# Optimization experiments

Measured on AMD Instinct MI355X. Metric: run time of the kernel, lower is better.

Reference implementation:

```python
import jax, jax.numpy as jnp
import numpy as np

IN_F, HID, OUT_F = 227, 1024, 227
BATCH, SEQ_LEN = 256, 100
COND_NUM, GT_NUM = 5, 5


def _condition_lst(seq_len, condition_num=COND_NUM, groundtruth_num=GT_NUM):
    gt = np.ones((100, groundtruth_num))
    con = np.zeros((100, condition_num))
    lst = np.concatenate((gt, con), 1).reshape(-1)
    return lst[:seq_len].astype(bool)


def _lstm_cell(x, h, c, Wih, Whh, bih, bhh):
    gates = x @ Wih.T + bih + h @ Whh.T + bhh  # [B, 4H]
    i, f, g, o = jnp.split(gates, 4, axis=-1)
    c_new = jax.nn.sigmoid(f) * c + jax.nn.sigmoid(i) * jnp.tanh(g)
    h_new = jax.nn.sigmoid(o) * jnp.tanh(c_new)
    return h_new, c_new


def setup_inputs() -> dict:
    key = jax.random.key(0)
    ks = jax.random.split(key, 16)
    s = 0.03
    inp = {"real_seq": jax.random.normal(ks[0], (BATCH, SEQ_LEN, IN_F), jnp.float32)}
    shapes = {
        "Wih1": (4 * HID, IN_F), "Whh1": (4 * HID, HID), "bih1": (4 * HID,), "bhh1": (4 * HID,),
        "Wih2": (4 * HID, HID), "Whh2": (4 * HID, HID), "bih2": (4 * HID,), "bhh2": (4 * HID,),
        "Wih3": (4 * HID, HID), "Whh3": (4 * HID, HID), "bih3": (4 * HID,), "bhh3": (4 * HID,),
        "Wd": (OUT_F, HID), "bd": (OUT_F,),
    }
    for i, (name, shp) in enumerate(shapes.items()):
        inp[name] = jax.random.normal(ks[i + 1], shp, jnp.float32) * s
    return inp


def reference(real_seq, Wih1, Whh1, bih1, bhh1, Wih2, Whh2, bih2, bhh2,
              Wih3, Whh3, bih3, bhh3, Wd, bd):
    batch, seq_len, _ = real_seq.shape
    cond = jnp.asarray(_condition_lst(seq_len))  # [T] bool, True -> teacher forcing
    zeros_h = jnp.zeros((batch, HID), real_seq.dtype)
    out0 = jnp.zeros((batch, OUT_F), real_seq.dtype)
    carry0 = (zeros_h, zeros_h, zeros_h, zeros_h, zeros_h, zeros_h, out0)

    def step(carry, xs):
        h0, h1, h2, c0, c1, c2, prev_out = carry
        gt_frame, use_gt = xs
        in_frame = jnp.where(use_gt, gt_frame, prev_out)
        # NOTE: faithful to the original quirk — lstm2/lstm3 consume the OLD
        # h0 / h1 (pre-update), not the freshly computed ones.
        h0n, c0n = _lstm_cell(in_frame, h0, c0, Wih1, Whh1, bih1, bhh1)
        h1n, c1n = _lstm_cell(h0, h1, c1, Wih2, Whh2, bih2, bhh2)
        h2n, c2n = _lstm_cell(h1, h2, c2, Wih3, Whh3, bih3, bhh3)
        out_frame = h2n @ Wd.T + bd
        return (h0n, h1n, h2n, c0n, c1n, c2n, out_frame), out_frame

    xs = (jnp.transpose(real_seq, (1, 0, 2)), cond)  # [T,B,F], [T]
    _, out_frames = jax.lax.scan(step, carry0, xs)   # [T,B,OUT_F]
    out_seq = jnp.transpose(out_frames, (1, 0, 2)).reshape(batch, seq_len * OUT_F)
    return out_seq
```

## Files before the change

kernel.cpp:

```cpp
#include <hip/hip_runtime.h>
#include <cstdint>

typedef _Float16 f16;
typedef _Float16 f16x8 __attribute__((ext_vector_type(8)));
typedef float    f32x4 __attribute__((ext_vector_type(4)));

#define DINL __device__ __forceinline__

static constexpr int HID = 1024;
static constexpr int NG  = 4096;
static constexpr int BB  = 256;
static constexpr int TT  = 100;
static constexpr int KX  = 256;
static constexpr size_t MSZ = (size_t)NG * HID;

static constexpr size_t OFF_PACKW5 = 0;
static constexpr size_t OFF_W1D    = OFF_PACKW5 + 5*MSZ*2;
static constexpr size_t OFF_WIH1   = OFF_W1D   + MSZ*2;
static constexpr size_t OFF_WD     = OFF_WIH1  + (size_t)NG*KX*2;
static constexpr size_t OFF_XPAD   = OFF_WD    + (size_t)256*HID*2;
static constexpr size_t OFF_BIAS   = OFF_XPAD  + (size_t)TT*BB*KX*2;
static constexpr size_t OFF_C      = OFF_BIAS  + (size_t)4*NG*4;
static constexpr size_t OFF_HBUF   = OFF_C     + (size_t)3*BB*HID*4;
static constexpr size_t OFF_H2Z    = OFF_HBUF  + (size_t)4*BB*HID*2;
static constexpr size_t OFF_H2ALL  = OFF_H2Z   + (size_t)BB*HID*2;

DINL size_t fpo(int n, int k, int NCH){
  return ((((size_t)(n>>4)*NCH + (k>>6))*2 + ((k>>5)&1)) << 9)
       + ((size_t)((n&15) | (((k>>3)&3) << 4)) << 3) + (k&7);
}

DINL void async16(void* lds, const void* g){
  auto lp = reinterpret_cast<__attribute__((address_space(3))) unsigned int*>(
      reinterpret_cast<uintptr_t>(lds));
  auto gp = reinterpret_cast<const __attribute__((address_space(1))) unsigned int*>(
      reinterpret_cast<uintptr_t>(g));
  __builtin_amdgcn_global_load_lds(gp, lp, 16, 0, 0);
}

DINL f16x8 ldsr128(unsigned a){
  f16x8 r;
  asm volatile("ds_read_b128 %0, %1" : "=v"(r) : "v"(a));
  return r;
}

DINL f16x8 gload(const void* addr){
  f16x8 r;
  asm volatile("global_load_dwordx4 %0, %1, off"
    : "=v"(r) : "v"(addr));
  return r;
}

DINL f32x4 mfma8(f16x8 a, f16x8 b, f32x4 c){
  return __builtin_amdgcn_mfma_f32_16x16x32_f16(a, b, c, 0, 0, 0);
}

DINL float sigf(float x){
  x = fminf(fmaxf(x, -30.f), 30.f);
  return __fdividef(1.f, 1.f + __expf(-x));
}
DINL float tanh_fast(float x){
  x = fminf(fmaxf(x, -15.f), 15.f);
  float t = __expf(2.f*x);
  return __fdividef(t - 1.f, t + 1.f);
}


__global__ void k_pack5(const float* W0, const float* W1, const float* W2,
                        const float* W3, const float* W4, char* ws)
{
  f16* dst = (f16*)(ws + OFF_PACKW5);
  const int mat = blockIdx.y;
  const float* src = mat==0?W0 : mat==1?W1 : mat==2?W2 : mat==3?W3 : W4;
  int tid = blockIdx.x*256 + threadIdx.x;
  int n = tid >> 7, kc = tid & 127;
  int r = ((n&3) << 10) + (n >> 2);
  const float* s = src + (size_t)r*HID + kc*8;
  f16x8 o;
  #pragma unroll
  for (int i = 0; i < 8; i++) o[i] = (f16)s[i];
  int nt = n >> 4, cch = kc >> 3, kw = (kc >> 2) & 1, quad = kc & 3;
  size_t off = ((((size_t)nt*16 + cch)*2 + kw) << 9)
             + ((size_t)((n&15) | (quad<<4)) << 3);
  *(f16x8*)(dst + (size_t)mat*MSZ + off) = o;
}

__global__ void k_packwih1(const float* __restrict__ Wih1, char* ws){
  f16* dst = (f16*)(ws + OFF_WIH1);
  int n = blockIdx.x, k = threadIdx.x;
  int r = ((n&3) << 10) + (n >> 2);
  dst[fpo(n, k, 4)] = (k < 227) ? (f16)Wih1[(size_t)r*227 + k] : (f16)0.f;
}

__global__ void k_packwd(const float* __restrict__ Wd, char* ws){
  f16* dst = (f16*)(ws + OFF_WD);
  int idx = blockIdx.x*256 + threadIdx.x;
  int o = idx >> 7, k8 = idx & 127;
  f16x8 v;
  #pragma unroll
  for (int e = 0; e < 8; e++)
    v[e] = (o < 227) ? (f16)Wd[(size_t)o*HID + k8*8 + e] : (f16)0.f;
  size_t off = ((((size_t)(o>>4)*16 + (k8>>3))*2 + ((k8>>2)&1)) << 9)
             + ((size_t)((o&15) | ((k8&3)<<4)) << 3);
  *(f16x8*)(dst + off) = v;
}

__global__ void k_packwdt(const float* __restrict__ Wd, char* ws){
  f16* dst = (f16*)(ws + OFF_H2ALL);
  int h = blockIdx.x, o = threadIdx.x;
  dst[fpo(h, o, 4)] = (o < 227) ? (f16)Wd[(size_t)o*HID + h] : (f16)0.f;
}

__global__ void k_xpad(const float* __restrict__ seq, char* ws){
  f16* dst = (f16*)(ws + OFF_XPAD);
  int idx = blockIdx.x*256 + threadIdx.x;
  int t = idx >> 13, rem = idx & 8191, b = rem >> 5, k8 = rem & 31;
  f16x8 v;
  #pragma unroll
  for (int e = 0; e < 8; e++){
    int k = k8*8 + e;
    v[e] = (k < 227) ? (f16)seq[(size_t)b*22700 + (size_t)t*227 + k] : (f16)0.f;
  }
  size_t off = ((((size_t)(b>>4)*4 + (k8>>3))*2 + ((k8>>2)&1)) << 9)
             + ((size_t)((b&15) | ((k8&3)<<4)) << 3);
  *(f16x8*)(dst + (size_t)t*BB*KX + off) = v;
}

__global__ void k_bias(const float* bih1, const float* bhh1, const float* bih2, const float* bhh2,
                       const float* bih3, const float* bhh3, const float* Wih1, const float* bd,
                       char* ws)
{
  int n = blockIdx.x*256 + threadIdx.x;
  if (n >= NG) return;
  int r = ((n&3) << 10) + (n >> 2);
  float* b = (float*)(ws + OFF_BIAS);
  float bf = bih1[r] + bhh1[r];
  float s = 0.f;
  for (int o = 0; o < 227; o++) s += Wih1[(size_t)r*227 + o] * bd[o];
  b[n]        = bf;
  b[NG + n]   = bf + s;
  b[2*NG + n] = bih2[r] + bhh2[r];
  b[3*NG + n] = bih3[r] + bhh3[r];
}

__global__ __launch_bounds__(256) void k_w1d(char* ws)
{
  const int w = threadIdx.x >> 6, lane = threadIdx.x & 63;
  const int n0 = blockIdx.x*128, m0 = blockIdx.y*128;
  const f16* Af = (const f16*)(ws + OFF_WIH1);
  const f16* Bf = (const f16*)(ws + OFF_H2ALL);
  f16* W1D = (f16*)(ws + OFF_W1D);
  const int m_w = m0 + (w>>1)*64, n_w = n0 + (w&1)*64;
  const int vl = lane*8;

  f32x4 acc[4][4];
  f32x4 zero = {0.f, 0.f, 0.f, 0.f};
  #pragma unroll
  for (int i = 0; i < 4; i++)
    #pragma unroll
    for (int j = 0; j < 4; j++) acc[i][j] = zero;

  for (int c = 0; c < 4; c++){
    f16x8 av[4][2], bv[4][2];
    #pragma unroll
    for (int ti = 0; ti < 4; ti++)
      #pragma unroll
      for (int kw = 0; kw < 2; kw++)
        av[ti][kw] = *(const f16x8*)(Af + ((((size_t)((m_w>>4)+ti)*4 + c)*2 + kw) << 9) + vl);
    #pragma unroll
    for (int tj = 0; tj < 4; tj++)
      #pragma unroll
      for (int kw = 0; kw < 2; kw++)
        bv[tj][kw] = *(const f16x8*)(Bf + ((((size_t)((n_w>>4)+tj)*4 + c)*2 + kw) << 9) + vl);
    #pragma unroll
    for (int kw = 0; kw < 2; kw++)
      #pragma unroll
      for (int ti = 0; ti < 4; ti++)
        #pragma unroll
        for (int tj = 0; tj < 4; tj++)
          acc[ti][tj] = mfma8(av[ti][kw], bv[tj][kw], acc[ti][tj]);
  }

  const int quad = lane>>4, c15 = lane&15;
  #pragma unroll
  for (int tj = 0; tj < 4; tj++){
    int col = n_w + tj*16 + c15;
    #pragma unroll
    for (int ti = 0; ti < 4; ti++){
      f32x4 v = acc[ti][tj];
      #pragma unroll
      for (int r = 0; r < 4; r++){
        int m = m_w + ti*16 + quad*4 + r;
        W1D[fpo(m, col, 16)] = (f16)v[r];
      }
    }
  }
}

__global__ __launch_bounds__(512, 2) void k_step(char* __restrict__ ws, int t, int use_gt)
{
  __shared__ __align__(16) char lds[65536];
  const int w = threadIdx.x >> 6, lane = threadIdx.x & 63;
  const int col0 = blockIdx.x*64, layer = blockIdx.y;

  const f16* packW = (const f16*)(ws + OFF_PACKW5);
  const f16* W1D   = (const f16*)(ws + OFF_W1D);
  const f16* WIH1  = (const f16*)(ws + OFF_WIH1);
  const f16* XP    = (const f16*)(ws + OFF_XPAD) + (size_t)t*BB*KX;
  const float* biasb = (const float*)(ws + OFF_BIAS);
  float* Cst = (float*)(ws + OFF_C);
  f16* HB  = (f16*)(ws + OFF_HBUF);
  f16* H2Z = (f16*)(ws + OFF_H2Z);
  f16* H2A = (f16*)(ws + OFF_H2ALL);

  const int pr = t & 1, pw = pr ^ 1;
  const f16* h0p = HB + (size_t)(pr*2 + 0)*BB*HID;
  const f16* h1p = HB + (size_t)(pr*2 + 1)*BB*HID;
  const f16* h2p = (t == 0) ? H2Z : (H2A + (size_t)(t-1)*BB*HID);

  const f16 *A0, *A1, *B0, *B1; int K1;
  const float* biasp; f16* hout; float* cptr;
  if (layer == 0){
    A0 = h0p; B0 = packW;
    if (use_gt){ A1 = XP;  B1 = WIH1; K1 = KX;  biasp = biasb; }
    else       { A1 = h2p; B1 = W1D;  K1 = HID; biasp = biasb + NG; }
    hout = HB + (size_t)(pw*2 + 0)*BB*HID; cptr = Cst;
  } else if (layer == 1){
    A0 = h0p; B0 = packW + MSZ;  A1 = h1p; B1 = packW + 2*MSZ; K1 = HID;
    biasp = biasb + 2*NG; hout = HB + (size_t)(pw*2 + 1)*BB*HID; cptr = Cst + (size_t)BB*HID;
  } else {
    A0 = h1p; B0 = packW + 3*MSZ; A1 = h2p; B1 = packW + 4*MSZ; K1 = HID;
    biasp = biasb + 3*NG; hout = H2A + (size_t)t*BB*HID; cptr = Cst + (size_t)2*BB*HID;
  }
  const int ncmax = 16 + (K1 >> 6);
  const int NCH1  = K1 >> 6;

  const int m_w = w*32, c15 = lane&15, quad = lane>>4;
  const unsigned vl16 = (unsigned)(lane * 16);
  const unsigned ldsBase = (unsigned)(uintptr_t)lds;

  const char* a0b[2]; const char* a1b[2];
  #pragma unroll
  for (int ti = 0; ti < 2; ti++){
    a0b[ti] = (const char*)A0 + (size_t)(2*w + ti)*16*2048   + (size_t)lane*16;
    a1b[ti] = (const char*)A1 + (size_t)(2*w + ti)*NCH1*2048 + (size_t)lane*16;
  }
  const char* b0u = (const char*)B0 + (size_t)((col0>>4) + (w>>1))*16*2048   + (size_t)(w&1)*1024 + (size_t)lane*16;
  const char* b1u = (const char*)B1 + (size_t)((col0>>4) + (w>>1))*NCH1*2048 + (size_t)(w&1)*1024 + (size_t)lane*16;

  auto issueB = [&](int ci){
    const char* s = (ci < 16) ? (b0u + (size_t)ci*2048) : (b1u + (size_t)(ci-16)*2048);
    async16(lds + (ci & 7)*8192 + w*1024, s);
  };
  auto abase = [&](int ci, int ti)->const char*{
    return (ci < 16) ? (a0b[ti] + (size_t)ci*2048) : (a1b[ti] + (size_t)(ci-16)*2048);
  };

  f32x4 acc[2][4];
  f32x4 zero = {0.f, 0.f, 0.f, 0.f};
  #pragma unroll
  for (int i = 0; i < 2; i++)
    #pragma unroll
    for (int j = 0; j < 4; j++) acc[i][j] = zero;

  f16x8 akA[4], akB[4];

#define ISSUEA(CI, AK)                                           \
  { const char* _b0 = abase((CI), 0);                            \
    const char* _b1 = abase((CI), 1);                            \
    AK[0] = gload(_b0);                                          \
    AK[1] = gload(_b0 + 1024);                                   \
    AK[2] = gload(_b1);                                          \
    AK[3] = gload(_b1 + 1024); }

#define WAITA(N, AK) asm volatile("s_waitcnt vmcnt(" #N ")"      \
    : "+v"(AK[0]), "+v"(AK[1]), "+v"(AK[2]), "+v"(AK[3]))

#define BMM(CI, AK)                                              \
  { const unsigned sb = ldsBase + (unsigned)(((CI)&7)*8192) + vl16; \
    f16x8 b00 = ldsr128(sb);        f16x8 b10 = ldsr128(sb+2048);   \
    f16x8 b20 = ldsr128(sb+4096);   f16x8 b30 = ldsr128(sb+6144);   \
    f16x8 b01 = ldsr128(sb+1024);   f16x8 b11 = ldsr128(sb+3072);   \
    f16x8 b21 = ldsr128(sb+5120);   f16x8 b31 = ldsr128(sb+7168);   \
    asm volatile("s_waitcnt lgkmcnt(4)"                          \
      : "+v"(b00), "+v"(b10), "+v"(b20), "+v"(b30));             \
    acc[0][0] = mfma8(AK[0], b00, acc[0][0]);                    \
    acc[0][1] = mfma8(AK[0], b10, acc[0][1]);                    \
    acc[0][2] = mfma8(AK[0], b20, acc[0][2]);                    \
    acc[0][3] = mfma8(AK[0], b30, acc[0][3]);                    \
    acc[1][0] = mfma8(AK[2], b00, acc[1][0]);                    \
    acc[1][1] = mfma8(AK[2], b10, acc[1][1]);                    \
    acc[1][2] = mfma8(AK[2], b20, acc[1][2]);                    \
    acc[1][3] = mfma8(AK[2], b30, acc[1][3]);                    \
    asm volatile("s_waitcnt lgkmcnt(0)"                          \
      : "+v"(b01), "+v"(b11), "+v"(b21), "+v"(b31));             \
    acc[0][0] = mfma8(AK[1], b01, acc[0][0]);                    \
    acc[0][1] = mfma8(AK[1], b11, acc[0][1]);                    \
    acc[0][2] = mfma8(AK[1], b21, acc[0][2]);                    \
    acc[0][3] = mfma8(AK[1], b31, acc[0][3]);                    \
    acc[1][0] = mfma8(AK[3], b01, acc[1][0]);                    \
    acc[1][1] = mfma8(AK[3], b11, acc[1][1]);                    \
    acc[1][2] = mfma8(AK[3], b21, acc[1][2]);                    \
    acc[1][3] = mfma8(AK[3], b31, acc[1][3]); }

#define ITERI(CI, VMN, AK)  { WAITA(VMN, AK); BMM(CI, AK); ISSUEA((CI)+2, AK); }
#define ITERN(CI, VMN, AK)  { WAITA(VMN, AK); BMM(CI, AK); }

  issueB(0); issueB(1); issueB(2); issueB(3);
  issueB(4); issueB(5); issueB(6); issueB(7);
  ISSUEA(0, akA); ISSUEA(1, akB);
  asm volatile("s_waitcnt vmcnt(4)" ::: "memory");
  __builtin_amdgcn_s_barrier();
  __builtin_amdgcn_sched_barrier(0);

  ITERI(0, 4, akA) ITERI(1, 4, akB) ITERI(2, 4, akA) ITERI(3, 4, akB)

  for (int h = 1; h <= (ncmax >> 2) - 2; ++h){
    __builtin_amdgcn_s_barrier();
    __builtin_amdgcn_sched_barrier(0);
    const int cb = 4*(h+1);
    issueB(cb); issueB(cb+1); issueB(cb+2); issueB(cb+3);
    const int c = 4*h;
    ITERI(c,   8, akA) ITERI(c+1, 8, akB) ITERI(c+2, 4, akA) ITERI(c+3, 4, akB)
  }

  __builtin_amdgcn_s_barrier();
  __builtin_amdgcn_sched_barrier(0);
  { const int c = ncmax - 4;
    ITERI(c,   4, akA) ITERI(c+1, 4, akB) ITERN(c+2, 4, akA) ITERN(c+3, 0, akB) }

#undef ITERN
#undef ITERI
#undef BMM
#undef WAITA
#undef ISSUEA

  const int gl = lane&3, sbase = lane&60;
  #pragma unroll
  for (int tj = 0; tj < 4; tj++){
    const int ncol = col0 + tj*16 + c15;
    const int unit = ncol >> 2;
    const float bn = biasp[ncol];
    float cp[8];
    #pragma unroll
    for (int ti = 0; ti < 2; ti++)
      #pragma unroll
      for (int r = 0; r < 4; r++)
        cp[ti*4 + r] = cptr[(size_t)(m_w + ti*16 + quad*4 + r)*HID + unit];
    #pragma unroll
    for (int ti = 0; ti < 2; ti++){
      f32x4 v = acc[ti][tj];
      #pragma unroll
      for (int r = 0; r < 4; r++){
        float x   = v[r] + bn;
        float act = (gl == 2) ? tanh_fast(x) : sigf(x);
        float iv = __shfl(act, sbase);
        float fv = __shfl(act, sbase + 1);
        float gv = __shfl(act, sbase + 2);
        float ov = __shfl(act, sbase + 3);
        float cn = fmaf(fv, cp[ti*4 + r], iv*gv);
        float hn = ov * tanh_fast(cn);
        int m = m_w + ti*16 + quad*4 + r;
        if (gl == 0)      cptr[(size_t)m*HID + unit] = cn;
        else if (gl == 1) hout[fpo(m, unit, 16)] = (f16)hn;
      }
    }
  }
}

__global__ __launch_bounds__(256) void k_final(const char* __restrict__ ws,
                                               const float* __restrict__ bd,
                                               float* __restrict__ dout)
{
  const int w = threadIdx.x >> 6, lane = threadIdx.x & 63;
  const int n0 = blockIdx.x*128, m0 = blockIdx.y*128;
  const char* Bf = ws + OFF_WD;
  const int m_w = m0 + (w>>1)*64, n_w = n0 + (w&1)*64;
  const char* Af = ws + OFF_H2ALL + (size_t)(m_w >> 8)*BB*HID*2;
  const int vl = lane*16;

  f32x4 acc[4][4];
  f32x4 zero = {0.f, 0.f, 0.f, 0.f};
  #pragma unroll
  for (int i = 0; i < 4; i++)
    #pragma unroll
    for (int j = 0; j < 4; j++) acc[i][j] = zero;

  for (int c = 0; c < 16; c++){
    f16x8 av[4][2], bv[4][2];
    #pragma unroll
    for (int ti = 0; ti < 4; ti++){
      const char* b = Af + (((size_t)(((m_w & 255) >> 4) + ti)*16 + c) << 11) + vl;
      av[ti][0] = *(const f16x8*)(b);
      av[ti][1] = *(const f16x8*)(b + 1024);
    }
    #pragma unroll
    for (int tj = 0; tj < 4; tj++){
      const char* b = Bf + (((size_t)((n_w >> 4) + tj)*16 + c) << 11) + vl;
      bv[tj][0] = *(const f16x8*)(b);
      bv[tj][1] = *(const f16x8*)(b + 1024);
    }
    #pragma unroll
    for (int kw = 0; kw < 2; kw++)
      #pragma unroll
      for (int ti = 0; ti < 4; ti++)
        #pragma unroll
        for (int tj = 0; tj < 4; tj++)
          acc[ti][tj] = mfma8(av[ti][kw], bv[tj][kw], acc[ti][tj]);
  }

  const int quad = lane>>4, c15 = lane&15;
  #pragma unroll
  for (int tj = 0; tj < 4; tj++){
    int o = n_w + tj*16 + c15;
    bool valid = (o < 227);
    float bn = valid ? bd[o] : 0.f;
    #pragma unroll
    for (int ti = 0; ti < 4; ti++){
      f32x4 v = acc[ti][tj];
      #pragma unroll
      for (int r = 0; r < 4; r++){
        int m = m_w + ti*16 + quad*4 + r;
        if (valid){
          int tt = m >> 8, b = m & 255;
          dout[(size_t)b*22700 + (size_t)tt*227 + o] = v[r] + bn;
        }
      }
    }
  }
}

extern "C" void kernel_launch(void* const* d_in, const int* in_sizes, int n_in,
                              void* d_out, int out_size, void* d_ws, size_t ws_size,
                              hipStream_t stream)
{
  (void)in_sizes; (void)n_in; (void)out_size; (void)ws_size;
  const float* seq  = (const float*)d_in[0];
  const float* Wih1 = (const float*)d_in[1];
  const float* Whh1 = (const float*)d_in[2];
  const float* bih1 = (const float*)d_in[3];
  const float* bhh1 = (const float*)d_in[4];
  const float* Wih2 = (const float*)d_in[5];
  const float* Whh2 = (const float*)d_in[6];
  const float* bih2 = (const float*)d_in[7];
  const float* bhh2 = (const float*)d_in[8];
  const float* Wih3 = (const float*)d_in[9];
  const float* Whh3 = (const float*)d_in[10];
  const float* bih3 = (const float*)d_in[11];
  const float* bhh3 = (const float*)d_in[12];
  const float* Wd   = (const float*)d_in[13];
  const float* bd   = (const float*)d_in[14];
  char* ws = (char*)d_ws;

  (void)hipMemsetAsync(ws + OFF_C,    0, (size_t)3*BB*HID*4, stream);
  (void)hipMemsetAsync(ws + OFF_HBUF, 0, (size_t)2*BB*HID*2, stream);
  (void)hipMemsetAsync(ws + OFF_H2Z,  0, (size_t)BB*HID*2,   stream);

  k_pack5   <<<dim3(2048, 5), dim3(256), 0, stream>>>(Whh1, Wih2, Whh2, Wih3, Whh3, ws);
  k_packwih1<<<dim3(4096),    dim3(256), 0, stream>>>(Wih1, ws);
  k_packwd  <<<dim3(128),     dim3(256), 0, stream>>>(Wd, ws);
  k_packwdt <<<dim3(1024),    dim3(256), 0, stream>>>(Wd, ws);
  k_xpad    <<<dim3(3200),    dim3(256), 0, stream>>>(seq, ws);
  k_bias    <<<dim3(16),      dim3(256), 0, stream>>>(bih1, bhh1, bih2, bhh2, bih3, bhh3, Wih1, bd, ws);
  k_w1d     <<<dim3(8, 32),   dim3(256), 0, stream>>>(ws);

  for (int t = 0; t < TT; t++){
    int ug = ((t % 10) < 5) ? 1 : 0;
    k_step<<<dim3(64, 3), dim3(512), 0, stream>>>(ws, t, ug);
  }

  k_final<<<dim3(2, 200), dim3(256), 0, stream>>>((const char*)ws, bd, (float*)d_out);
}
```

Before: 2.918 ms.

## Deepen GEMM pipeline with triple-buffered A registers and prefetched LDS B fragments

Restructures the recurrent GEMM main loop so A fragments are loaded three chunks ahead (three register sets instead of two) and B fragments for the next chunk are read from LDS into a second register set while the MFMAs for the current chunk run. The loop is unrolled into 12-chunk blocks with barriers and B async copies placed every four chunks. The aim is to hide global-load and LDS-read latency behind the MFMAs. In exchange it raises VGPR pressure, which may lower occupancy, and the hand-counted waitcnt values make it fragile if ncmax-8 is not a multiple of 12.

```diff
diff --git a/kernel.cpp b/kernel.cpp
--- a/kernel.cpp
+++ b/kernel.cpp
@@ -263,7 +263,8 @@
     #pragma unroll
     for (int j = 0; j < 4; j++) acc[i][j] = zero;
 
-  f16x8 akA[4], akB[4];
+  f16x8 A0r[4], A1r[4], A2r[4];
+  f16x8 F0[8], F1[8];
 
 #define ISSUEA(CI, AK)                                           \
   { const char* _b0 = abase((CI), 0);                            \
@@ -273,66 +274,84 @@
     AK[2] = gload(_b1);                                          \
     AK[3] = gload(_b1 + 1024); }
 
-#define WAITA(N, AK) asm volatile("s_waitcnt vmcnt(" #N ")"      \
+#define WAITA_N(LIT, AK) asm volatile("s_waitcnt vmcnt(" #LIT ")" \
     : "+v"(AK[0]), "+v"(AK[1]), "+v"(AK[2]), "+v"(AK[3]))
 
-#define BMM(CI, AK)                                              \
-  { const unsigned sb = ldsBase + (unsigned)(((CI)&7)*8192) + vl16; \
-    f16x8 b00 = ldsr128(sb);        f16x8 b10 = ldsr128(sb+2048);   \
-    f16x8 b20 = ldsr128(sb+4096);   f16x8 b30 = ldsr128(sb+6144);   \
-    f16x8 b01 = ldsr128(sb+1024);   f16x8 b11 = ldsr128(sb+3072);   \
-    f16x8 b21 = ldsr128(sb+5120);   f16x8 b31 = ldsr128(sb+7168);   \
-    asm volatile("s_waitcnt lgkmcnt(4)"                          \
-      : "+v"(b00), "+v"(b10), "+v"(b20), "+v"(b30));             \
-    acc[0][0] = mfma8(AK[0], b00, acc[0][0]);                    \
-    acc[0][1] = mfma8(AK[0], b10, acc[0][1]);                    \
-    acc[0][2] = mfma8(AK[0], b20, acc[0][2]);                    \
-    acc[0][3] = mfma8(AK[0], b30, acc[0][3]);                    \
-    acc[1][0] = mfma8(AK[2], b00, acc[1][0]);                    \
-    acc[1][1] = mfma8(AK[2], b10, acc[1][1]);                    \
-    acc[1][2] = mfma8(AK[2], b20, acc[1][2]);                    \
-    acc[1][3] = mfma8(AK[2], b30, acc[1][3]);                    \
-    asm volatile("s_waitcnt lgkmcnt(0)"                          \
-      : "+v"(b01), "+v"(b11), "+v"(b21), "+v"(b31));             \
-    acc[0][0] = mfma8(AK[1], b01, acc[0][0]);                    \
-    acc[0][1] = mfma8(AK[1], b11, acc[0][1]);                    \
-    acc[0][2] = mfma8(AK[1], b21, acc[0][2]);                    \
-    acc[0][3] = mfma8(AK[1], b31, acc[0][3]);                    \
-    acc[1][0] = mfma8(AK[3], b01, acc[1][0]);                    \
-    acc[1][1] = mfma8(AK[3], b11, acc[1][1]);                    \
-    acc[1][2] = mfma8(AK[3], b21, acc[1][2]);                    \
-    acc[1][3] = mfma8(AK[3], b31, acc[1][3]); }
-
-#define ITERI(CI, VMN, AK)  { WAITA(VMN, AK); BMM(CI, AK); ISSUEA((CI)+2, AK); }
-#define ITERN(CI, VMN, AK)  { WAITA(VMN, AK); BMM(CI, AK); }
-
-  issueB(0); issueB(1); issueB(2); issueB(3);
-  issueB(4); issueB(5); issueB(6); issueB(7);
-  ISSUEA(0, akA); ISSUEA(1, akB);
-  asm volatile("s_waitcnt vmcnt(4)" ::: "memory");
-  __builtin_amdgcn_s_barrier();
-  __builtin_amdgcn_sched_barrier(0);
-
-  ITERI(0, 4, akA) ITERI(1, 4, akB) ITERI(2, 4, akA) ITERI(3, 4, akB)
-
-  for (int h = 1; h <= (ncmax >> 2) - 2; ++h){
-    __builtin_amdgcn_s_barrier();
-    __builtin_amdgcn_sched_barrier(0);
-    const int cb = 4*(h+1);
-    issueB(cb); issueB(cb+1); issueB(cb+2); issueB(cb+3);
-    const int c = 4*h;
-    ITERI(c,   8, akA) ITERI(c+1, 8, akB) ITERI(c+2, 4, akA) ITERI(c+3, 4, akB)
-  }
-
-  __builtin_amdgcn_s_barrier();
-  __builtin_amdgcn_sched_barrier(0);
-  { const int c = ncmax - 4;
-    ITERI(c,   4, akA) ITERI(c+1, 4, akB) ITERN(c+2, 4, akA) ITERN(c+3, 0, akB) }
-
-#undef ITERN
-#undef ITERI
-#undef BMM
-#undef WAITA
+#define DS8(CI, F)                                               \
+  { const unsigned _sb = ldsBase + (unsigned)(((CI)&7)*8192) + vl16; \
+    F[0] = ldsr128(_sb);         F[1] = ldsr128(_sb + 1024u);    \
+    F[2] = ldsr128(_sb + 2048u); F[3] = ldsr128(_sb + 3072u);    \
+    F[4] = ldsr128(_sb + 4096u); F[5] = ldsr128(_sb + 5120u);    \
+    F[6] = ldsr128(_sb + 6144u); F[7] = ldsr128(_sb + 7168u); }
+
+#define LGKM_N(LIT, F) asm volatile("s_waitcnt lgkmcnt(" #LIT ")" \
+    : "+v"(F[0]), "+v"(F[1]), "+v"(F[2]), "+v"(F[3]),            \
+      "+v"(F[4]), "+v"(F[5]), "+v"(F[6]), "+v"(F[7]))
+
+#define MFMA16(AK, F)                                            \
+    acc[0][0] = mfma8(AK[0], F[0], acc[0][0]);                   \
+    acc[0][1] = mfma8(AK[0], F[2], acc[0][1]);                   \
+    acc[0][2] = mfma8(AK[0], F[4], acc[0][2]);                   \
+    acc[0][3] = mfma8(AK[0], F[6], acc[0][3]);                   \
+    acc[1][0] = mfma8(AK[2], F[0], acc[1][0]);                   \
+    acc[1][1] = mfma8(AK[2], F[2], acc[1][1]);                   \
+    acc[1][2] = mfma8(AK[2], F[4], acc[1][2]);                   \
+    acc[1][3] = mfma8(AK[2], F[6], acc[1][3]);                   \
+    acc[0][0] = mfma8(AK[1], F[1], acc[0][0]);                   \
+    acc[0][1] = mfma8(AK[1], F[3], acc[0][1]);                   \
+    acc[0][2] = mfma8(AK[1], F[5], acc[0][2]);                   \
+    acc[0][3] = mfma8(AK[1], F[7], acc[0][3]);                   \
+    acc[1][0] = mfma8(AK[3], F[1], acc[1][0]);                   \
+    acc[1][1] = mfma8(AK[3], F[3], acc[1][1]);                   \
+    acc[1][2] = mfma8(AK[3], F[5], acc[1][2]);                   \
+    acc[1][3] = mfma8(AK[3], F[7], acc[1][3]);
+
+#define BARRIER_ { __builtin_amdgcn_s_barrier(); __builtin_amdgcn_sched_barrier(0); }
+#define ISSUEB4(G) { const int _cb = 4*(G); issueB(_cb); issueB(_cb+1); issueB(_cb+2); issueB(_cb+3); }
+
+  ISSUEB4(0); ISSUEB4(1);
+  ISSUEA(0, A0r); ISSUEA(1, A1r); ISSUEA(2, A2r);
+  asm volatile("s_waitcnt vmcnt(16)" ::: "memory");
+  BARRIER_;
+  DS8(0, F0);
+
+  WAITA_N(8, A0r); DS8(1, F1); LGKM_N(8, F0); MFMA16(A0r, F0); ISSUEA(3, A0r);
+  WAITA_N(8, A1r); DS8(2, F0); LGKM_N(8, F1); MFMA16(A1r, F1); ISSUEA(4, A1r);
+  WAITA_N(8, A2r); DS8(3, F1); LGKM_N(8, F0); MFMA16(A2r, F0); ISSUEA(5, A2r);
+
+  const int nblk = (ncmax - 8) / 12;
+  for (int blk = 0; blk < nblk; ++blk){
+    const int c0 = 3 + 12*blk, g0 = c0 >> 2;
+    LGKM_N(0, F1); BARRIER_; ISSUEB4(g0+2);
+    WAITA_N(12, A0r); DS8(c0+1, F0); MFMA16(A0r, F1); ISSUEA(c0+3, A0r);
+    WAITA_N(12, A1r); DS8(c0+2, F1); LGKM_N(8, F0); MFMA16(A1r, F0); ISSUEA(c0+4,  A1r);
+    WAITA_N(12, A2r); DS8(c0+3, F0); LGKM_N(8, F1); MFMA16(A2r, F1); ISSUEA(c0+5,  A2r);
+    WAITA_N(8,  A0r); DS8(c0+4, F1); LGKM_N(8, F0); MFMA16(A0r, F0); ISSUEA(c0+6,  A0r);
+    LGKM_N(0, F1); BARRIER_; ISSUEB4(g0+3);
+    WAITA_N(12, A1r); DS8(c0+5, F0); MFMA16(A1r, F1); ISSUEA(c0+7, A1r);
+    WAITA_N(12, A2r); DS8(c0+6, F1); LGKM_N(8, F0); MFMA16(A2r, F0); ISSUEA(c0+8,  A2r);
+    WAITA_N(12, A0r); DS8(c0+7, F0); LGKM_N(8, F1); MFMA16(A0r, F1); ISSUEA(c0+9,  A0r);
+    WAITA_N(8,  A1r); DS8(c0+8, F1); LGKM_N(8, F0); MFMA16(A1r, F0); ISSUEA(c0+10, A1r);
+    LGKM_N(0, F1); BARRIER_; ISSUEB4(g0+4);
+    WAITA_N(12, A2r); DS8(c0+9, F0); MFMA16(A2r, F1); ISSUEA(c0+11, A2r);
+    WAITA_N(12, A0r); DS8(c0+10, F1); LGKM_N(8, F0); MFMA16(A0r, F0); ISSUEA(c0+12, A0r);
+    WAITA_N(12, A1r); DS8(c0+11, F0); LGKM_N(8, F1); MFMA16(A1r, F1); ISSUEA(c0+13, A1r);
+    WAITA_N(8,  A2r); DS8(c0+12, F1); LGKM_N(8, F0); MFMA16(A2r, F0); ISSUEA(c0+14, A2r);
+  }
+
+  LGKM_N(0, F1); BARRIER_;
+  WAITA_N(8, A0r); DS8(ncmax-4, F0); MFMA16(A0r, F1); ISSUEA(ncmax-2, A0r);
+  WAITA_N(8, A1r); DS8(ncmax-3, F1); LGKM_N(8, F0); MFMA16(A1r, F0); ISSUEA(ncmax-1, A1r);
+  WAITA_N(8, A2r); DS8(ncmax-2, F0); LGKM_N(8, F1); MFMA16(A2r, F1);
+  WAITA_N(4, A0r); DS8(ncmax-1, F1); LGKM_N(8, F0); MFMA16(A0r, F0);
+  WAITA_N(0, A1r);                   LGKM_N(0, F1); MFMA16(A1r, F1);
+
+#undef ISSUEB4
+#undef BARRIER_
+#undef MFMA16
+#undef LGKM_N
+#undef DS8
+#undef WAITA_N
 #undef ISSUEA
 
   const int gl = lane&3, sbase = lane&60;
```

Result: no change. 2.880 ms (-1.3%).
